# Kernel tuning notes

Measured on AMD Instinct MI355X. Metric: run time of the kernel, lower is better.

Reference implementation:

```python
import jax, jax.numpy as jnp
import numpy as np

B, DIM, HID = 16384, 512, 256
DT, N_STEPS = 0.1, 3


def setup_inputs() -> dict:
    key = jax.random.key(0)
    ks = jax.random.split(key, 5)
    z = jax.random.normal(ks[0], (B, DIM), dtype=jnp.float32)
    # HNN energy MLP: 2*DIM -> HID -> HID -> 1 (tanh activations)
    s1 = 1.0 / np.sqrt(2 * DIM)
    s2 = 1.0 / np.sqrt(HID)
    W1 = jax.random.normal(ks[1], (2 * DIM, HID), dtype=jnp.float32) * s1
    b1 = jnp.zeros((HID,), dtype=jnp.float32)
    W2 = jax.random.normal(ks[2], (HID, HID), dtype=jnp.float32) * s2
    b2 = jnp.zeros((HID,), dtype=jnp.float32)
    W3 = jax.random.normal(ks[3], (HID, 1), dtype=jnp.float32) * s2
    b3 = jnp.zeros((1,), dtype=jnp.float32)
    return {"z": z, "W1": W1, "b1": b1, "W2": W2, "b2": b2, "W3": W3, "b3": b3}


def reference(z, W1, b1, W2, b2, W3, b3):
    d = z.shape[-1]
    dt = jnp.float32(DT)

    def H_sum(zp):  # total Hamiltonian over the batch -> scalar
        h = jnp.tanh(zp @ W1 + b1)
        h = jnp.tanh(h @ W2 + b2)
        return jnp.sum(h @ W3 + b3)

    gradH = jax.grad(H_sum)  # [B, 2d]: (dH/dq, dH/dp) per sample

    def leapfrog(zp):
        q, p = zp[:, :d], zp[:, d:]
        # half-step momentum: dp/dt = -dH/dq
        g = gradH(jnp.concatenate([q, p], axis=-1))
        p = p - 0.5 * dt * g[:, :d]
        # full-step position: dq/dt = dH/dp
        g = gradH(jnp.concatenate([q, p], axis=-1))
        q = q + dt * g[:, d:]
        # half-step momentum
        g = gradH(jnp.concatenate([q, p], axis=-1))
        p = p - 0.5 * dt * g[:, :d]
        return jnp.concatenate([q, p], axis=-1)

    zp = jnp.concatenate([z, jnp.zeros_like(z)], axis=-1)  # phase space [B, 2d]
    for _ in range(N_STEPS):  # fixed small unroll (n_steps=3)
        zp = leapfrog(zp)
    return zp[:, :d]
```

## Files before the change

### kernel.cpp

```cpp
#include <hip/hip_runtime.h>
#include <math.h>

#define DT 0.1f

typedef __attribute__((ext_vector_type(4)))  short short4v;
typedef __attribute__((ext_vector_type(8)))  short short8;
typedef __attribute__((ext_vector_type(16))) float f32x16;

__device__ __forceinline__ short f2bf(float x) {
    unsigned int u = __float_as_uint(x);
    unsigned int r = (u + 0x7fffu + ((u >> 16) & 1u)) >> 16;
    return (short)r;
}
__device__ __forceinline__ float bf2f(short s) {
    return __uint_as_float(((unsigned int)(unsigned short)s) << 16);
}
__device__ __forceinline__ float tanh_fast(float x) {
    float e = __expf(x + x);
    float r = __builtin_amdgcn_rcpf(e + 1.f);
    return __builtin_fmaf(-2.f, r, 1.f);
}

__device__ __forceinline__ void pack32_body(const float* __restrict__ W,
                                            short* __restrict__ out,
                                            int K, int N, int idx, bool trans)
{
    int j = idx & 7, lane = (idx >> 3) & 63, rest = idx >> 9;
    int KT = K >> 4;
    int kt = rest % KT, nt = rest / KT;
    int k = kt * 16 + (lane >> 5) * 8 + j;
    int n = nt * 32 + (lane & 31);
    out[idx] = f2bf(trans ? W[n * K + k] : W[k * N + n]);
}

__global__ __launch_bounds__(256)
void prep(const float* __restrict__ W1, const float* __restrict__ W2,
          const float* __restrict__ z,
          short* __restrict__ PBSq, short* __restrict__ PBSp,
          short* __restrict__ PB2, short* __restrict__ PB2T,
          short* __restrict__ PB1q, short* __restrict__ PB1Tp,
          short* __restrict__ zpA)
{
    __shared__ short zb[32 * 520];
    const int tid = threadIdx.x;
    const int b = blockIdx.x;

    if (b < 512) {
        const int n = tid;
        float s[8];
#pragma unroll
        for (int i = 0; i < 8; ++i) s[i] = 0.f;
        int k; float coef; short* dst;
        if (b < 256) {
            k = b; coef = -0.5f * DT; dst = PBSq;
            for (int c = 0; c < 512; c += 8) {
#pragma unroll
                for (int i = 0; i < 8; ++i)
                    s[i] = __builtin_fmaf(W1[(c + i) * 256 + k],
                                          W1[(512 + c + i) * 256 + n], s[i]);
            }
        } else {
            k = b - 256; coef = DT; dst = PBSp;
            for (int c = 0; c < 512; c += 8) {
#pragma unroll
                for (int i = 0; i < 8; ++i)
                    s[i] = __builtin_fmaf(W1[(512 + c + i) * 256 + k],
                                          W1[(c + i) * 256 + n], s[i]);
            }
        }
        float v = coef * (((s[0] + s[1]) + (s[2] + s[3])) +
                          ((s[4] + s[5]) + (s[6] + s[7])));
        int kt = k >> 4, r = k & 15;
        int lane = (r >> 3) * 32 + (n & 31), nt = n >> 5;
        dst[(((nt * 16 + kt) * 64 + lane) << 3) + (r & 7)] = f2bf(v);
    } else if (b < 768) {
        pack32_body(W2, PB2, 256, 256, (b - 512) * 256 + tid, false);
    } else if (b < 1024) {
        pack32_body(W2, PB2T, 256, 256, (b - 768) * 256 + tid, true);
    } else if (b < 1536) {
        pack32_body(W1, PB1q, 512, 256, (b - 1024) * 256 + tid, false);
    } else if (b < 2048) {
        pack32_body(W1 + 512 * 256, PB1Tp, 256, 512, (b - 1536) * 256 + tid, true);
    } else {
        const int bx = b - 2048;
#pragma unroll
        for (int j = 0; j < 16; ++j) {
            int lin = j * 256 + tid;
            int r = lin >> 7, c4 = lin & 127;
            float4 v = ((const float4*)z)[(size_t)(bx * 32 + r) * 128 + c4];
            short4v pk;
            pk.x = f2bf(v.x); pk.y = f2bf(v.y); pk.z = f2bf(v.z); pk.w = f2bf(v.w);
            *(short4v*)&zb[r * 520 + c4 * 4] = pk;
        }
        __syncthreads();
        const int lane = tid & 63, w = tid >> 6;
        const int m = lane & 31, lh = lane >> 5;
#pragma unroll
        for (int j = 0; j < 8; ++j) {
            int kt = w * 8 + j;
            short8 f = *(const short8*)&zb[m * 520 + kt * 16 + lh * 8];
            *(short8*)(zpA + (((size_t)bx * 32 + kt) * 64 + lane) * 8) = f;
        }
    }
}

__device__ __forceinline__ short8 lds_frag32(const short* Ac, int kt,
                                             int l31, int lh, int rot)
{
    int nt_s = kt >> 1;
    int po = (((kt & 1) * 2 + lh) * 4 + rot) & 15;
    int base = (nt_s * 64 + l31) * 16 + po;
    short4v x = *(const short4v*)&Ac[base];
    short4v y = *(const short4v*)&Ac[base + 512];
    short8 r;
    r[0] = x.x; r[1] = x.y; r[2] = x.z; r[3] = x.w;
    r[4] = y.x; r[5] = y.y; r[6] = y.z; r[7] = y.w;
    return r;
}
__device__ __forceinline__ void store_tile32(short* Ac, int nt, int lane,
                                             int rot, const f32x16 v)
{
    int base = (nt * 64 + lane) * 16;
#pragma unroll
    for (int c = 0; c < 4; ++c) {
        short4v pk;
        pk.x = f2bf(v[4 * c + 0]); pk.y = f2bf(v[4 * c + 1]);
        pk.z = f2bf(v[4 * c + 2]); pk.w = f2bf(v[4 * c + 3]);
        *(short4v*)&Ac[base + ((4 * c + rot) & 15)] = pk;
    }
}

__device__ __forceinline__ void gemm_nt32(const short* Ac, int l31, int lh, int rot,
                                          const short8* __restrict__ Bf, f32x16& acc)
{
    short8 pb[8];
#pragma unroll
    for (int k = 0; k < 8; ++k) pb[k] = Bf[k * 64];
    short8 pa0 = lds_frag32(Ac, 0, l31, lh, rot);
    short8 pa1 = lds_frag32(Ac, 1, l31, lh, rot);
#pragma unroll
    for (int kt = 0; kt < 16; ++kt) {
        short8 ca = pa0, cb = pb[kt & 7];
        pa0 = pa1;
        if (kt + 2 < 16) pa1 = lds_frag32(Ac, kt + 2, l31, lh, rot);
        if (kt + 8 < 16) pb[kt & 7] = Bf[(kt + 8) * 64];
        acc = __builtin_amdgcn_mfma_f32_32x32x16_bf16(ca, cb, acc, 0, 0, 0);
    }
}

__global__ __launch_bounds__(512, 2)
void mega(const short* __restrict__ zpA,
          const short* __restrict__ PB1q,
          const short* __restrict__ PB2,
          const short* __restrict__ PB2T,
          const short* __restrict__ PBSq,
          const short* __restrict__ PBSp,
          const float* __restrict__ b1,
          const float* __restrict__ b2,
          const float* __restrict__ W3,
          const short* __restrict__ PB1Tp,
          const float* __restrict__ z,
          float* __restrict__ out)
{
    __shared__ alignas(16) short smem[16384];
    short* h1_c = smem;
    short* da_c = smem + 8192;

    const int tid = threadIdx.x;
    const int lane = tid & 63, w = tid >> 6;
    const int l31 = lane & 31, lh = lane >> 5;
    const int rot = ((l31 >> 2) & 3) * 4;
    const int bx = blockIdx.x;

    const int col = w * 32 + l31;
    const float b1v = b1[col], b2v = b2[col], w3v = W3[col];

    f32x16 A1 = 0.f;
    f32x16 dsum = 0.f;

    {
        const short8* Af = (const short8*)zpA + ((size_t)bx * 32) * 64 + lane;
        const short8* Bf = (const short8*)PB1q + ((size_t)w * 32) * 64 + lane;
        short8 pa[4], pb[8];
#pragma unroll
        for (int k = 0; k < 4; ++k) pa[k] = Af[k * 64];
#pragma unroll
        for (int k = 0; k < 8; ++k) pb[k] = Bf[k * 64];
#pragma unroll
        for (int kt = 0; kt < 32; ++kt) {
            short8 ca = pa[kt & 3], cb = pb[kt & 7];
            if (kt + 4 < 32) pa[kt & 3] = Af[(kt + 4) * 64];
            if (kt + 8 < 32) pb[kt & 7] = Bf[(kt + 8) * 64];
            A1 = __builtin_amdgcn_mfma_f32_32x32x16_bf16(ca, cb, A1, 0, 0, 0);
        }
    }

    for (int it = 0; it < 8; ++it) {
        const bool isq = ((it % 3) == 1);

        {
            f32x16 hv;
#pragma unroll
            for (int r = 0; r < 16; ++r) hv[r] = tanh_fast(A1[r] + b1v);
            store_tile32(h1_c, w, lane, rot, hv);
        }
        __syncthreads();

        {
            f32x16 t0 = 0.f;
            gemm_nt32(h1_c, l31, lh, rot,
                      (const short8*)PB2 + ((size_t)w * 16) * 64 + lane, t0);
            f32x16 d;
#pragma unroll
            for (int r = 0; r < 16; ++r) {
                float ta = tanh_fast(t0[r] + b2v);
                d[r] = w3v * (1.f - ta * ta);
            }
            store_tile32(da_c, w, lane, rot, d);
        }
        __syncthreads();

        {
            f32x16 t0 = 0.f;
            gemm_nt32(da_c, l31, lh, rot,
                      (const short8*)PB2T + ((size_t)w * 16) * 64 + lane, t0);
            __syncthreads();
            f32x16 d;
            const int basei = (w * 64 + lane) * 16;
#pragma unroll
            for (int c = 0; c < 4; ++c) {
                short4v h4 = *(const short4v*)&h1_c[basei + ((4 * c + rot) & 15)];
                float h0 = bf2f(h4.x), h1f = bf2f(h4.y);
                float h2 = bf2f(h4.z), h3 = bf2f(h4.w);
                d[4 * c + 0] = t0[4 * c + 0] * (1.f - h0 * h0);
                d[4 * c + 1] = t0[4 * c + 1] * (1.f - h1f * h1f);
                d[4 * c + 2] = t0[4 * c + 2] * (1.f - h2 * h2);
                d[4 * c + 3] = t0[4 * c + 3] * (1.f - h3 * h3);
            }
            if (isq) dsum += d;
            store_tile32(da_c, w, lane, rot, d);
        }
        __syncthreads();

        if (it < 7) {
            const short* S = isq ? PBSp : PBSq;
            gemm_nt32(da_c, l31, lh, rot,
                      (const short8*)S + ((size_t)w * 16) * 64 + lane, A1);
        }
    }

    store_tile32(da_c, w, lane, rot, dsum);
    __syncthreads();

    f32x16 acc2[2];
    acc2[0] = 0.f; acc2[1] = 0.f;
    {
        const short8* Bf0 = (const short8*)PB1Tp + (size_t)(2 * w + 0) * 16 * 64 + lane;
        const short8* Bf1 = (const short8*)PB1Tp + (size_t)(2 * w + 1) * 16 * 64 + lane;
        short8 pb0[4], pb1[4];
#pragma unroll
        for (int k = 0; k < 4; ++k) { pb0[k] = Bf0[k * 64]; pb1[k] = Bf1[k * 64]; }
        short8 pa0 = lds_frag32(da_c, 0, l31, lh, rot);
        short8 pa1 = lds_frag32(da_c, 1, l31, lh, rot);
#pragma unroll
        for (int kt = 0; kt < 16; ++kt) {
            short8 ca = pa0, cb0 = pb0[kt & 3], cb1 = pb1[kt & 3];
            pa0 = pa1;
            if (kt + 2 < 16) pa1 = lds_frag32(da_c, kt + 2, l31, lh, rot);
            if (kt + 4 < 16) {
                pb0[kt & 3] = Bf0[(kt + 4) * 64];
                pb1[kt & 3] = Bf1[(kt + 4) * 64];
            }
            acc2[0] = __builtin_amdgcn_mfma_f32_32x32x16_bf16(ca, cb0, acc2[0], 0, 0, 0);
            acc2[1] = __builtin_amdgcn_mfma_f32_32x32x16_bf16(ca, cb1, acc2[1], 0, 0, 0);
        }
    }
    __syncthreads();

    float* Ct = (float*)smem;
#pragma unroll
    for (int p = 0; p < 2; ++p) {
        if ((w >> 2) == p) {
#pragma unroll
            for (int t = 0; t < 2; ++t) {
                const int cl = (w & 3) * 64 + t * 32 + l31;
#pragma unroll
                for (int r = 0; r < 16; ++r) {
                    int row = (r & 3) + 8 * (r >> 2) + 4 * lh;
                    Ct[row * 256 + cl] = acc2[t][r];
                }
            }
        }
        __syncthreads();
#pragma unroll
        for (int j = 0; j < 4; ++j) {
            int lin = j * 512 + tid;
            int r = lin >> 6, c4 = lin & 63;
            size_t gi = (size_t)(bx * 32 + r) * 128 + p * 64 + c4;
            float4 zv = ((const float4*)z)[gi];
            float4 cv = *(const float4*)&Ct[r * 256 + c4 * 4];
            float4 ov;
            ov.x = zv.x + DT * cv.x; ov.y = zv.y + DT * cv.y;
            ov.z = zv.z + DT * cv.z; ov.w = zv.w + DT * cv.w;
            ((float4*)out)[gi] = ov;
        }
        __syncthreads();
    }
}

extern "C" void kernel_launch(void* const* d_in, const int* in_sizes, int n_in,
                              void* d_out, int out_size, void* d_ws, size_t ws_size,
                              hipStream_t stream)
{
    const float* z  = (const float*)d_in[0];
    const float* W1 = (const float*)d_in[1];
    const float* b1 = (const float*)d_in[2];
    const float* W2 = (const float*)d_in[3];
    const float* b2 = (const float*)d_in[4];
    const float* W3 = (const float*)d_in[5];
    float* out = (float*)d_out;

    short* PB2   = (short*)d_ws;
    short* PB2T  = PB2   + 65536;
    short* PBSq  = PB2T  + 65536;
    short* PBSp  = PBSq  + 65536;
    short* PB1q  = PBSp  + 65536;
    short* PB1Tp = PB1q  + 131072;
    short* zpA   = PB1Tp + 131072;

    prep<<<2560, 256, 0, stream>>>(W1, W2, z, PBSq, PBSp, PB2, PB2T,
                                   PB1q, PB1Tp, zpA);
    mega<<<512, 512, 0, stream>>>(zpA, PB1q, PB2, PB2T, PBSq, PBSp,
                                  b1, b2, W3, PB1Tp, z, out);
}
```

Before: 200.8 us.

## Process 64 rows per block with 1024 threads sharing weight tiles

Each block now handles two 32-row M tiles with 16 waves (8 column tiles by 2 row tiles), so 256 blocks of 1024 threads replace 512 blocks of 512. The aim is to let two waves share each weight column slice through L2 and cut the grid in half. The B-fragment prefetch depth drops from 8 to 4 to save registers. Risks: 1024-thread barriers cost more, there are fewer blocks to spread across the CUs, and the LDS footprint doubles to 64KB per block.

Result: slower. 298.4 us (+48.6%).

```diff
diff --git a/kernel.cpp b/kernel.cpp
--- a/kernel.cpp
+++ b/kernel.cpp
@@ -104,12 +104,12 @@
     }
 }
 
-__device__ __forceinline__ short8 lds_frag32(const short* Ac, int kt,
-                                             int l31, int lh, int rot)
+__device__ __forceinline__ short8 lds_frag(const short* Ac, int kt, int mt2,
+                                           int l31, int lh, int rot)
 {
     int nt_s = kt >> 1;
     int po = (((kt & 1) * 2 + lh) * 4 + rot) & 15;
-    int base = (nt_s * 64 + l31) * 16 + po;
+    int base = ((nt_s * 2 + mt2) * 64 + l31) * 16 + po;
     short4v x = *(const short4v*)&Ac[base];
     short4v y = *(const short4v*)&Ac[base + 512];
     short8 r;
@@ -117,10 +117,10 @@
     r[4] = y.x; r[5] = y.y; r[6] = y.z; r[7] = y.w;
     return r;
 }
-__device__ __forceinline__ void store_tile32(short* Ac, int nt, int lane,
-                                             int rot, const f32x16 v)
-{
-    int base = (nt * 64 + lane) * 16;
+__device__ __forceinline__ void store_tile(short* Ac, int nt, int mt2, int lane,
+                                           int rot, const f32x16 v)
+{
+    int base = ((nt * 2 + mt2) * 64 + lane) * 16;
 #pragma unroll
     for (int c = 0; c < 4; ++c) {
         short4v pk;
@@ -130,25 +130,26 @@
     }
 }
 
-__device__ __forceinline__ void gemm_nt32(const short* Ac, int l31, int lh, int rot,
-                                          const short8* __restrict__ Bf, f32x16& acc)
-{
-    short8 pb[8];
-#pragma unroll
-    for (int k = 0; k < 8; ++k) pb[k] = Bf[k * 64];
-    short8 pa0 = lds_frag32(Ac, 0, l31, lh, rot);
-    short8 pa1 = lds_frag32(Ac, 1, l31, lh, rot);
+__device__ __forceinline__ void gemm16(const short* Ac, int mt2, int l31, int lh,
+                                       int rot, const short8* __restrict__ Bf,
+                                       f32x16& acc)
+{
+    short8 pb[4];
+#pragma unroll
+    for (int k = 0; k < 4; ++k) pb[k] = Bf[k * 64];
+    short8 pa0 = lds_frag(Ac, 0, mt2, l31, lh, rot);
+    short8 pa1 = lds_frag(Ac, 1, mt2, l31, lh, rot);
 #pragma unroll
     for (int kt = 0; kt < 16; ++kt) {
-        short8 ca = pa0, cb = pb[kt & 7];
+        short8 ca = pa0, cb = pb[kt & 3];
         pa0 = pa1;
-        if (kt + 2 < 16) pa1 = lds_frag32(Ac, kt + 2, l31, lh, rot);
-        if (kt + 8 < 16) pb[kt & 7] = Bf[(kt + 8) * 64];
+        if (kt + 2 < 16) pa1 = lds_frag(Ac, kt + 2, mt2, l31, lh, rot);
+        if (kt + 4 < 16) pb[kt & 3] = Bf[(kt + 4) * 64];
         acc = __builtin_amdgcn_mfma_f32_32x32x16_bf16(ca, cb, acc, 0, 0, 0);
     }
 }
 
-__global__ __launch_bounds__(512, 2)
+__global__ __launch_bounds__(1024, 1)
 void mega(const short* __restrict__ zpA,
           const short* __restrict__ PB1q,
           const short* __restrict__ PB2,
@@ -162,35 +163,36 @@
           const float* __restrict__ z,
           float* __restrict__ out)
 {
-    __shared__ alignas(16) short smem[16384];
+    __shared__ alignas(16) short smem[32768];
     short* h1_c = smem;
-    short* da_c = smem + 8192;
+    short* da_c = smem + 16384;
 
     const int tid = threadIdx.x;
     const int lane = tid & 63, w = tid >> 6;
+    const int nt = w & 7, mt2 = w >> 3;
     const int l31 = lane & 31, lh = lane >> 5;
     const int rot = ((l31 >> 2) & 3) * 4;
     const int bx = blockIdx.x;
 
-    const int col = w * 32 + l31;
+    const int col = nt * 32 + l31;
     const float b1v = b1[col], b2v = b2[col], w3v = W3[col];
 
     f32x16 A1 = 0.f;
     f32x16 dsum = 0.f;
 
     {
-        const short8* Af = (const short8*)zpA + ((size_t)bx * 32) * 64 + lane;
-        const short8* Bf = (const short8*)PB1q + ((size_t)w * 32) * 64 + lane;
-        short8 pa[4], pb[8];
-#pragma unroll
-        for (int k = 0; k < 4; ++k) pa[k] = Af[k * 64];
-#pragma unroll
-        for (int k = 0; k < 8; ++k) pb[k] = Bf[k * 64];
+        const short8* Af = (const short8*)zpA + ((size_t)(bx * 2 + mt2) * 32) * 64 + lane;
+        const short8* Bf = (const short8*)PB1q + ((size_t)nt * 32) * 64 + lane;
+        short8 pa[4], pb[4];
+#pragma unroll
+        for (int k = 0; k < 4; ++k) { pa[k] = Af[k * 64]; pb[k] = Bf[k * 64]; }
 #pragma unroll
         for (int kt = 0; kt < 32; ++kt) {
-            short8 ca = pa[kt & 3], cb = pb[kt & 7];
-            if (kt + 4 < 32) pa[kt & 3] = Af[(kt + 4) * 64];
-            if (kt + 8 < 32) pb[kt & 7] = Bf[(kt + 8) * 64];
+            short8 ca = pa[kt & 3], cb = pb[kt & 3];
+            if (kt + 4 < 32) {
+                pa[kt & 3] = Af[(kt + 4) * 64];
+                pb[kt & 3] = Bf[(kt + 4) * 64];
+            }
             A1 = __builtin_amdgcn_mfma_f32_32x32x16_bf16(ca, cb, A1, 0, 0, 0);
         }
     }
@@ -202,31 +204,31 @@
             f32x16 hv;
 #pragma unroll
             for (int r = 0; r < 16; ++r) hv[r] = tanh_fast(A1[r] + b1v);
-            store_tile32(h1_c, w, lane, rot, hv);
+            store_tile(h1_c, nt, mt2, lane, rot, hv);
         }
         __syncthreads();
 
         {
             f32x16 t0 = 0.f;
-            gemm_nt32(h1_c, l31, lh, rot,
-                      (const short8*)PB2 + ((size_t)w * 16) * 64 + lane, t0);
+            gemm16(h1_c, mt2, l31, lh, rot,
+                   (const short8*)PB2 + ((size_t)nt * 16) * 64 + lane, t0);
             f32x16 d;
 #pragma unroll
             for (int r = 0; r < 16; ++r) {
                 float ta = tanh_fast(t0[r] + b2v);
                 d[r] = w3v * (1.f - ta * ta);
             }
-            store_tile32(da_c, w, lane, rot, d);
+            store_tile(da_c, nt, mt2, lane, rot, d);
         }
         __syncthreads();
 
         {
             f32x16 t0 = 0.f;
-            gemm_nt32(da_c, l31, lh, rot,
-                      (const short8*)PB2T + ((size_t)w * 16) * 64 + lane, t0);
+            gemm16(da_c, mt2, l31, lh, rot,
+                   (const short8*)PB2T + ((size_t)nt * 16) * 64 + lane, t0);
             __syncthreads();
             f32x16 d;
-            const int basei = (w * 64 + lane) * 16;
+            const int basei = ((nt * 2 + mt2) * 64 + lane) * 16;
 #pragma unroll
             for (int c = 0; c < 4; ++c) {
                 short4v h4 = *(const short4v*)&h1_c[basei + ((4 * c + rot) & 15)];
@@ -238,35 +240,35 @@
                 d[4 * c + 3] = t0[4 * c + 3] * (1.f - h3 * h3);
             }
             if (isq) dsum += d;
-            store_tile32(da_c, w, lane, rot, d);
+            store_tile(da_c, nt, mt2, lane, rot, d);
         }
         __syncthreads();
 
         if (it < 7) {
             const short* S = isq ? PBSp : PBSq;
-            gemm_nt32(da_c, l31, lh, rot,
-                      (const short8*)S + ((size_t)w * 16) * 64 + lane, A1);
-        }
-    }
-
-    store_tile32(da_c, w, lane, rot, dsum);
+            gemm16(da_c, mt2, l31, lh, rot,
+                   (const short8*)S + ((size_t)nt * 16) * 64 + lane, A1);
+        }
+    }
+
+    store_tile(da_c, nt, mt2, lane, rot, dsum);
     __syncthreads();
 
     f32x16 acc2[2];
     acc2[0] = 0.f; acc2[1] = 0.f;
     {
-        const short8* Bf0 = (const short8*)PB1Tp + (size_t)(2 * w + 0) * 16 * 64 + lane;
-        const short8* Bf1 = (const short8*)PB1Tp + (size_t)(2 * w + 1) * 16 * 64 + lane;
+        const short8* Bf0 = (const short8*)PB1Tp + (size_t)(2 * nt + 0) * 16 * 64 + lane;
+        const short8* Bf1 = (const short8*)PB1Tp + (size_t)(2 * nt + 1) * 16 * 64 + lane;
         short8 pb0[4], pb1[4];
 #pragma unroll
         for (int k = 0; k < 4; ++k) { pb0[k] = Bf0[k * 64]; pb1[k] = Bf1[k * 64]; }
-        short8 pa0 = lds_frag32(da_c, 0, l31, lh, rot);
-        short8 pa1 = lds_frag32(da_c, 1, l31, lh, rot);
+        short8 pa0 = lds_frag(da_c, 0, mt2, l31, lh, rot);
+        short8 pa1 = lds_frag(da_c, 1, mt2, l31, lh, rot);
 #pragma unroll
         for (int kt = 0; kt < 16; ++kt) {
             short8 ca = pa0, cb0 = pb0[kt & 3], cb1 = pb1[kt & 3];
             pa0 = pa1;
-            if (kt + 2 < 16) pa1 = lds_frag32(da_c, kt + 2, l31, lh, rot);
+            if (kt + 2 < 16) pa1 = lds_frag(da_c, kt + 2, mt2, l31, lh, rot);
             if (kt + 4 < 16) {
                 pb0[kt & 3] = Bf0[(kt + 4) * 64];
                 pb1[kt & 3] = Bf1[(kt + 4) * 64];
@@ -280,25 +282,25 @@
     float* Ct = (float*)smem;
 #pragma unroll
     for (int p = 0; p < 2; ++p) {
-        if ((w >> 2) == p) {
+        if (mt2 == p) {
 #pragma unroll
             for (int t = 0; t < 2; ++t) {
-                const int cl = (w & 3) * 64 + t * 32 + l31;
+                const int c = (nt * 2 + t) * 32 + l31;
 #pragma unroll
                 for (int r = 0; r < 16; ++r) {
                     int row = (r & 3) + 8 * (r >> 2) + 4 * lh;
-                    Ct[row * 256 + cl] = acc2[t][r];
+                    Ct[row * 512 + c] = acc2[t][r];
                 }
             }
         }
         __syncthreads();
 #pragma unroll
         for (int j = 0; j < 4; ++j) {
-            int lin = j * 512 + tid;
-            int r = lin >> 6, c4 = lin & 63;
-            size_t gi = (size_t)(bx * 32 + r) * 128 + p * 64 + c4;
+            int lin = j * 1024 + tid;
+            int r = lin >> 7, c4 = lin & 127;
+            size_t gi = (size_t)(bx * 64 + p * 32 + r) * 128 + c4;
             float4 zv = ((const float4*)z)[gi];
-            float4 cv = *(const float4*)&Ct[r * 256 + c4 * 4];
+            float4 cv = *(const float4*)&Ct[r * 512 + c4 * 4];
             float4 ov;
             ov.x = zv.x + DT * cv.x; ov.y = zv.y + DT * cv.y;
             ov.z = zv.z + DT * cv.z; ov.w = zv.w + DT * cv.w;
@@ -330,6 +332,6 @@
 
     prep<<<2560, 256, 0, stream>>>(W1, W2, z, PBSq, PBSp, PB2, PB2T,
                                    PB1q, PB1Tp, zpA);
-    mega<<<512, 512, 0, stream>>>(zpA, PB1q, PB2, PB2T, PBSq, PBSp,
-                                  b1, b2, W3, PB1Tp, z, out);
-}
+    mega<<<256, 1024, 0, stream>>>(zpA, PB1q, PB2, PB2T, PBSq, PBSp,
+                                   b1, b2, W3, PB1Tp, z, out);
+}
```
